# Optimization experiments

Measured on AMD Instinct MI355X. Metric: run time of the kernel, lower is better.

Reference implementation:

```python
import jax, jax.numpy as jnp
import numpy as np

D_IN = 2048
D_OUT = 2048
NUM_HEADS = 16
HEAD_DIM = D_OUT // NUM_HEADS
CONTEXT_LENGTH = 4096
THETA_BASE = 10000.0


def _rope_tables(seq_len):
    half = HEAD_DIM // 2
    inv_freq = 1.0 / (THETA_BASE ** (jnp.arange(half, dtype=jnp.float32) / half))
    positions = jnp.arange(seq_len, dtype=jnp.float32)
    angles = positions[:, None] * inv_freq[None, :]          # [S, half]
    angles = jnp.concatenate([angles, angles], axis=-1)      # [S, HEAD_DIM]
    return jnp.cos(angles), jnp.sin(angles)


def _apply_rope(x, cos, sin):
    # x: [B, H, S, D]
    half = x.shape[-1] // 2
    x1, x2 = x[..., :half], x[..., half:]
    rotated = jnp.concatenate([-x2, x1], axis=-1)
    return x * cos[None, None, :, :] + rotated * sin[None, None, :, :]


def setup_inputs() -> dict:
    key = jax.random.key(0)
    ks = jax.random.split(key, 5)
    x = jax.random.normal(ks[0], (1, 4096, D_IN), dtype=jnp.float32)
    scale_in = 1.0 / np.sqrt(D_IN)
    scale_out = 1.0 / np.sqrt(D_OUT)
    w_q = jax.random.normal(ks[1], (D_OUT, D_IN), dtype=jnp.float32) * scale_in
    w_k = jax.random.normal(ks[2], (D_OUT, D_IN), dtype=jnp.float32) * scale_in
    w_v = jax.random.normal(ks[3], (D_OUT, D_IN), dtype=jnp.float32) * scale_in
    w_o = jax.random.normal(ks[4], (D_IN, D_OUT), dtype=jnp.float32) * scale_out
    return {"x": x, "w_q": w_q, "w_k": w_k, "w_v": w_v, "w_o": w_o}


def reference(x, w_q, w_k, w_v, w_o):
    b, s, _ = x.shape
    cos, sin = _rope_tables(s)

    def split_heads(t):  # [B,S,D_OUT] -> [B,H,S,HEAD_DIM]
        return t.reshape(b, s, NUM_HEADS, HEAD_DIM).transpose(0, 2, 1, 3)

    q = split_heads(jnp.einsum('bsd,od->bso', x, w_q))
    k = split_heads(jnp.einsum('bsd,od->bso', x, w_k))
    v = split_heads(jnp.einsum('bsd,od->bso', x, w_v))

    q = _apply_rope(q, cos, sin)
    k = _apply_rope(k, cos, sin)

    scores = jnp.einsum('bhqd,bhkd->bhqk', q, k) / jnp.sqrt(jnp.float32(HEAD_DIM))
    causal = jnp.tril(jnp.ones((s, s), dtype=bool))
    scores = jnp.where(causal[None, None, :, :], scores, -jnp.inf)
    attn = jax.nn.softmax(scores, axis=-1)

    ctx = jnp.einsum('bhqk,bhkd->bhqd', attn, v)  # [B,H,S,HEAD_DIM]
    ctx = ctx.transpose(0, 2, 1, 3).reshape(b, s, D_OUT)
    return jnp.einsum('bso,do->bsd', ctx, w_o)
```

## Files before the change

kernel.cpp:

```cpp
#include <hip/hip_runtime.h>
#include <hip/hip_bf16.h>
#include <stdint.h>

#define SEQ 4096
#define DM 2048
#define NH 16
#define HD 128

typedef __attribute__((ext_vector_type(4)))  float f32x4;
typedef __attribute__((ext_vector_type(16))) float f32x16;
typedef __attribute__((ext_vector_type(8)))  short bf16x8;
typedef __attribute__((ext_vector_type(4)))  float float4_t;
typedef __attribute__((ext_vector_type(4)))  short s16x4;
typedef __attribute__((ext_vector_type(2)))  int   i32x2;
typedef __attribute__((ext_vector_type(2)))  unsigned u32x2;

__device__ __forceinline__ short f2bf(float f) {
  union { float f; unsigned u; } c; c.f = f;
  unsigned u = c.u;
  u += 0x7FFFu + ((u >> 16) & 1u);
  return (short)(u >> 16);
}

__device__ __forceinline__ int cvtpk(float lo, float hi) {
  int r;
  asm("v_cvt_pk_bf16_f32 %0, %1, %2" : "=v"(r) : "v"(lo), "v"(hi));
  return r;
}

__device__ __forceinline__ void async16(const void* g, void* l) {
  __builtin_amdgcn_global_load_lds((const __attribute__((address_space(1))) void*)g,
                                   (__attribute__((address_space(3))) void*)l, 16, 0, 0);
}

__global__ __launch_bounds__(256) void rope_tables_kernel(float2* __restrict__ tab) {
  int idx = blockIdx.x * 256 + threadIdx.x;
  int s = idx >> 6, j = idx & 63;
  float invf = expf(-(float)j * (9.210340371976184f / 64.0f));
  float ang = (float)s * invf;
  tab[idx] = make_float2(cosf(ang), sinf(ang));
}

__global__ __launch_bounds__(256) void f32_to_bf16_kernel(const float* __restrict__ in,
                                                          short* __restrict__ out, int n4) {
  int stride = gridDim.x * 256;
  for (int i = blockIdx.x * 256 + threadIdx.x; i < n4; i += stride) {
    float4_t v = ((const float4_t*)in)[i];
    s16x4 r;
    #pragma unroll
    for (int u = 0; u < 4; u++) r[u] = f2bf(v[u]);
    ((s16x4*)out)[i] = r;
  }
}

template<int OUT_MODE>
__global__ __launch_bounds__(256) void gemm_async_kernel(
    const short* __restrict__ A, const short* __restrict__ B,
    void* __restrict__ Cp, int M, int N, int K) {
  __shared__ short As[128 * 64];
  __shared__ short Bs[128 * 64];
  const int t = threadIdx.x, lane = t & 63, w = t >> 6;
  const int wr = w >> 1, wc = w & 1;
  const size_t Mbase = (size_t)blockIdx.x * 128;
  const size_t Nbase = (size_t)blockIdx.y * 128;
  f32x4 acc[4][4] = {};

  for (int k0 = 0; k0 < K; k0 += 64) {
    __syncthreads();
    #pragma unroll
    for (int c = 0; c < 4; c++) {
      int ob = w * 4096 + c * 1024;
      int o = ob + lane * 16;
      int row = o >> 7;
      int cb = (o & 127) ^ ((row & 7) << 4);
      async16((const char*)A + ((Mbase + row) * (size_t)K + k0) * 2 + cb, (char*)As + ob);
      async16((const char*)B + ((Nbase + row) * (size_t)K + k0) * 2 + cb, (char*)Bs + ob);
    }
    __syncthreads();

    bf16x8 a[2][4], b[2][4];
    #pragma unroll
    for (int ks = 0; ks < 2; ks++) {
      #pragma unroll
      for (int m = 0; m < 4; m++) {
        int row = wr * 64 + m * 16 + (lane & 15);
        int chunk = ks * 64 + (lane >> 4) * 16;
        a[ks][m] = *(const bf16x8*)((const char*)As + row * 128 + (chunk ^ ((row & 7) << 4)));
      }
      #pragma unroll
      for (int n = 0; n < 4; n++) {
        int row = wc * 64 + n * 16 + (lane & 15);
        int chunk = ks * 64 + (lane >> 4) * 16;
        b[ks][n] = *(const bf16x8*)((const char*)Bs + row * 128 + (chunk ^ ((row & 7) << 4)));
      }
    }
    #pragma unroll
    for (int ks = 0; ks < 2; ks++)
      #pragma unroll
      for (int m = 0; m < 4; m++)
        #pragma unroll
        for (int n = 0; n < 4; n++)
          acc[m][n] = __builtin_amdgcn_mfma_f32_16x16x32_bf16(a[ks][m], b[ks][n], acc[m][n], 0, 0, 0);
  }

  #pragma unroll
  for (int m = 0; m < 4; m++)
    #pragma unroll
    for (int n = 0; n < 4; n++)
      #pragma unroll
      for (int j = 0; j < 4; j++) {
        size_t row = Mbase + wr * 64 + m * 16 + (lane >> 4) * 4 + j;
        size_t col = Nbase + wc * 64 + n * 16 + (lane & 15);
        float v = acc[m][n][j];
        if (OUT_MODE == 0) ((float*)Cp)[row * N + col] = v;
        else               ((short*)Cp)[col * (size_t)M + row] = f2bf(v);
      }
}

template<int IS_Q>
__global__ __launch_bounds__(256) void gemm_rope_kernel(
    const short* __restrict__ A, const short* __restrict__ B,
    short* __restrict__ C, const float2* __restrict__ tab) {
  __shared__ short As[128 * 64];
  __shared__ short Bs[128 * 64];
  const int t = threadIdx.x, lane = t & 63, w = t >> 6;
  const size_t Mbase = (size_t)blockIdx.x * 128;
  const size_t Nbase = (size_t)blockIdx.y * 128;
  const int K = DM;
  f32x4 acc[2][8] = {};

  for (int k0 = 0; k0 < K; k0 += 64) {
    __syncthreads();
    #pragma unroll
    for (int c = 0; c < 4; c++) {
      int ob = w * 4096 + c * 1024;
      int o = ob + lane * 16;
      int row = o >> 7;
      int cb = (o & 127) ^ ((row & 7) << 4);
      async16((const char*)A + ((Mbase + row) * (size_t)K + k0) * 2 + cb, (char*)As + ob);
      async16((const char*)B + ((Nbase + row) * (size_t)K + k0) * 2 + cb, (char*)Bs + ob);
    }
    __syncthreads();

    bf16x8 a[2][2], b[2][8];
    #pragma unroll
    for (int ks = 0; ks < 2; ks++) {
      #pragma unroll
      for (int m = 0; m < 2; m++) {
        int row = w * 32 + m * 16 + (lane & 15);
        int chunk = ks * 64 + (lane >> 4) * 16;
        a[ks][m] = *(const bf16x8*)((const char*)As + row * 128 + (chunk ^ ((row & 7) << 4)));
      }
      #pragma unroll
      for (int n = 0; n < 8; n++) {
        int row = n * 16 + (lane & 15);
        int chunk = ks * 64 + (lane >> 4) * 16;
        b[ks][n] = *(const bf16x8*)((const char*)Bs + row * 128 + (chunk ^ ((row & 7) << 4)));
      }
    }
    #pragma unroll
    for (int ks = 0; ks < 2; ks++)
      #pragma unroll
      for (int m = 0; m < 2; m++)
        #pragma unroll
        for (int n = 0; n < 8; n++)
          acc[m][n] = __builtin_amdgcn_mfma_f32_16x16x32_bf16(a[ks][m], b[ks][n], acc[m][n], 0, 0, 0);
  }

  const float SC = IS_Q ? 0.12751746f : 1.0f;
  #pragma unroll
  for (int m = 0; m < 2; m++)
    #pragma unroll
    for (int n = 0; n < 4; n++)
      #pragma unroll
      for (int j = 0; j < 4; j++) {
        int row = (int)Mbase + w * 32 + m * 16 + (lane >> 4) * 4 + j;
        int dj = n * 16 + (lane & 15);
        float2 cs = tab[row * 64 + dj];
        float cc = cs.x * SC, ss = cs.y * SC;
        float r1 = acc[m][n][j], r2 = acc[m][n + 4][j];
        C[(size_t)row * DM + Nbase + dj]      = f2bf(r1 * cc - r2 * ss);
        C[(size_t)row * DM + Nbase + dj + 64] = f2bf(r2 * cc + r1 * ss);
      }
}

__global__ __launch_bounds__(512) void flash_attn4_kernel(
    const short* __restrict__ Q, const short* __restrict__ K,
    const short* __restrict__ VT, short* __restrict__ O) {
  __shared__ __align__(16) char LB[132096];
  const int t = threadIdx.x, lane = t & 63, w = t >> 6;
  const int hi = lane >> 5, c31 = lane & 31;
  const int s = w & 3, v = w >> 2;
  const int id = blockIdx.x;
  const int h  = (id & 7) * 2 + ((id >> 3) & 1);
  const int pr = id >> 4;

  float* Opart = (float*)LB;
  float* ml    = (float*)(LB + 131072);

  auto stage = [&](int kt, int buf) {
    #pragma unroll
    for (int it = 0; it < 4; it++) {
      const int ob = w * 4096 + it * 1024;
      const int o  = ob + lane * 16;
      const int row = o >> 8;
      const int xs = (o & 255) ^ ((row & 15) << 4);
      async16((const char*)K + ((size_t)(kt * 128 + row) * DM + h * HD) * 2 + xs,
              LB + buf * 32768 + ob);
      async16((const char*)VT + ((size_t)(h * HD + row) * SEQ + (size_t)kt * 128) * 2 + xs,
              LB + 65536 + buf * 32768 + ob);
    }
  };

  for (int rep = 0; rep < 2; rep++) {
    const int qt = rep ? (31 - pr) : pr;
    const int q0 = qt * 128;
    const int nt = qt + 1;
    const int qrow = q0 + s * 32 + c31;

    __syncthreads();
    stage(0, 0);

    bf16x8 qf[8];
    #pragma unroll
    for (int ss = 0; ss < 8; ss++)
      qf[ss] = *(const bf16x8*)(Q + (size_t)qrow * DM + h * HD + ss * 16 + hi * 8);

    f32x16 oacc[4] = {};
    float m = -3.0e38f, l = 0.f;

    __syncthreads();

    for (int kt = 0; kt < nt; kt++) {
      const int buf = kt & 1;
      if (kt + 1 < nt) stage(kt + 1, buf ^ 1);

      if (kt * 128 + v * 64 <= q0 + s * 32 + 31) {
        const char* KsB = LB + buf * 32768;
        const char* VsB = LB + 65536 + buf * 32768;

        f32x16 sacc[2] = {};
        __builtin_amdgcn_s_setprio(1);
        #pragma unroll
        for (int a = 0; a < 2; a++)
          #pragma unroll
          for (int ss = 0; ss < 8; ss++) {
            int row = v * 64 + a * 32 + c31;
            bf16x8 kf = *(const bf16x8*)(KsB + row * 256
                                         + ((ss * 32 + hi * 16) ^ ((row & 15) << 4)));
            sacc[a] = __builtin_amdgcn_mfma_f32_32x32x16_bf16(kf, qf[ss], sacc[a], 0, 0, 0);
          }
        __builtin_amdgcn_s_setprio(0);

        float t0[16];
        #pragma unroll
        for (int r = 0; r < 16; r++) t0[r] = fmaxf(sacc[0][r], sacc[1][r]);
        #pragma unroll
        for (int d = 8; d > 0; d >>= 1)
          #pragma unroll
          for (int r = 0; r < 8; r++) if (r < d) t0[r] = fmaxf(t0[r], t0[r + d]);
        float mx = t0[0];
        i32x2 mm = __builtin_amdgcn_permlane32_swap(__float_as_int(mx), __float_as_int(mx),
                                                    false, false);
        mx = fmaxf(__int_as_float(mm.x), __int_as_float(mm.y));

        if (__any(mx > m + 11.5416f)) {
          float mn = fmaxf(m, mx);
          float al = exp2f(m - mn);
          m = mn; l *= al;
          #pragma unroll
          for (int g = 0; g < 4; g++)
            #pragma unroll
            for (int r = 0; r < 16; r++) oacc[g][r] *= al;
        }

        const int rel = qrow - kt * 128 - v * 64;
        const bool maskT = (kt * 128 + v * 64 + 63) > (q0 + s * 32);
        #pragma unroll
        for (int a = 0; a < 2; a++)
          #pragma unroll
          for (int r = 0; r < 16; r++) {
            float e = exp2f(sacc[a][r] - m);
            if (maskT) {
              int kl = a * 32 + (r & 3) + 8 * (r >> 2) + 4 * hi;
              e = (kl > rel) ? 0.f : e;
            }
            sacc[a][r] = e;
          }

        float s0[16];
        #pragma unroll
        for (int r = 0; r < 16; r++) s0[r] = sacc[0][r] + sacc[1][r];
        #pragma unroll
        for (int d = 8; d > 0; d >>= 1)
          #pragma unroll
          for (int r = 0; r < 8; r++) if (r < d) s0[r] = s0[r] + s0[r + d];
        l += s0[0];

        bf16x8 pa[4];
        #pragma unroll
        for (int a = 0; a < 2; a++)
          #pragma unroll
          for (int sg = 0; sg < 2; sg++) {
            int q0a = cvtpk(sacc[a][8 * sg + 0], sacc[a][8 * sg + 1]);
            int q1a = cvtpk(sacc[a][8 * sg + 2], sacc[a][8 * sg + 3]);
            int q0b = cvtpk(sacc[a][8 * sg + 4], sacc[a][8 * sg + 5]);
            int q1b = cvtpk(sacc[a][8 * sg + 6], sacc[a][8 * sg + 7]);
            i32x2 r0 = __builtin_amdgcn_permlane32_swap(q0a, q0b, false, false);
            i32x2 r1 = __builtin_amdgcn_permlane32_swap(q1a, q1b, false, false);
            union { int d[4]; bf16x8 vv; } u;
            u.d[0] = r0.x; u.d[1] = r1.x; u.d[2] = r0.y; u.d[3] = r1.y;
            pa[a * 2 + sg] = u.vv;
          }

        __builtin_amdgcn_s_setprio(1);
        #pragma unroll
        for (int ks = 0; ks < 4; ks++)
          #pragma unroll
          for (int g = 0; g < 4; g++) {
            int row = g * 32 + c31;
            bf16x8 vf = *(const bf16x8*)(VsB + row * 256
                         + (((v * 64 + ks * 16 + hi * 8) * 2) ^ ((row & 15) << 4)));
            oacc[g] = __builtin_amdgcn_mfma_f32_32x32x16_bf16(vf, pa[ks], oacc[g], 0, 0, 0);
          }
        __builtin_amdgcn_s_setprio(0);
      }
      __syncthreads();
    }

    i32x2 lr = __builtin_amdgcn_permlane32_swap(__float_as_int(l), __float_as_int(l),
                                                false, false);
    l = __int_as_float(lr.x) + __int_as_float(lr.y);

    if (v == 1) {
      #pragma unroll
      for (int g = 0; g < 4; g++)
        #pragma unroll
        for (int r = 0; r < 16; r++) {
          int d = g * 32 + (r & 3) + 8 * (r >> 2) + 4 * hi;
          Opart[s * 4096 + d * 32 + c31] = oacc[g][r];
        }
      if (hi == 0) {
        ml[(s * 32 + c31) * 2]     = m;
        ml[(s * 32 + c31) * 2 + 1] = l;
      }
    }
    __syncthreads();
    if (v == 0) {
      float lB = ml[(s * 32 + c31) * 2 + 1];
      float mB = (lB > 0.f) ? ml[(s * 32 + c31) * 2] : -3.0e38f;
      float ms = fmaxf(m, mB);
      float aA = exp2f(m - ms), aB = exp2f(mB - ms);
      float linv = 1.0f / (l * aA + lB * aB);
      float sA = aA * linv, sB = aB * linv;
      #pragma unroll
      for (int g = 0; g < 4; g++)
        #pragma unroll
        for (int tt = 0; tt < 4; tt++) {
          float o[4];
          #pragma unroll
          for (int e = 0; e < 4; e++) {
            int d = g * 32 + e + 8 * tt + 4 * hi;
            o[e] = oacc[g][4 * tt + e] * sA + Opart[s * 4096 + d * 32 + c31] * sB;
          }
          u32x2 pk;
          pk.x = (unsigned)cvtpk(o[0], o[1]);
          pk.y = (unsigned)cvtpk(o[2], o[3]);
          *(u32x2*)(O + (size_t)qrow * DM + h * HD + g * 32 + tt * 8 + hi * 4) = pk;
        }
    }
  }
}

extern "C" void kernel_launch(void* const* d_in, const int* in_sizes, int n_in,
                              void* d_out, int out_size, void* d_ws, size_t ws_size,
                              hipStream_t stream) {
  const float* x  = (const float*)d_in[0];
  const float* wq = (const float*)d_in[1];
  const float* wk = (const float*)d_in[2];
  const float* wv = (const float*)d_in[3];
  const float* wo = (const float*)d_in[4];
  float* out = (float*)d_out;

  const size_t SQDMs = (size_t)SEQ * DM;
  short* Qb   = (short*)d_ws;
  short* Kb   = Qb + SQDMs;
  short* VTb  = Kb + SQDMs;
  short* Cb   = VTb + SQDMs;
  short* xbf  = Cb + SQDMs;
  short* wbuf = xbf + SQDMs;
  float2* tab = (float2*)(wbuf + (size_t)DM * DM);

  rope_tables_kernel<<<SEQ * 64 / 256, 256, 0, stream>>>(tab);
  f32_to_bf16_kernel<<<2048, 256, 0, stream>>>(x, xbf, (int)(SQDMs / 4));

  dim3 g(SEQ / 128, DM / 128);
  f32_to_bf16_kernel<<<2048, 256, 0, stream>>>(wq, wbuf, DM * DM / 4);
  gemm_rope_kernel<1><<<g, 256, 0, stream>>>(xbf, wbuf, Qb, tab);
  f32_to_bf16_kernel<<<2048, 256, 0, stream>>>(wk, wbuf, DM * DM / 4);
  gemm_rope_kernel<0><<<g, 256, 0, stream>>>(xbf, wbuf, Kb, tab);
  f32_to_bf16_kernel<<<2048, 256, 0, stream>>>(wv, wbuf, DM * DM / 4);
  gemm_async_kernel<2><<<g, 256, 0, stream>>>(xbf, wbuf, VTb, SEQ, DM, DM);

  flash_attn4_kernel<<<256, 512, 0, stream>>>(Qb, Kb, VTb, Cb);

  f32_to_bf16_kernel<<<2048, 256, 0, stream>>>(wo, wbuf, DM * DM / 4);
  gemm_async_kernel<0><<<g, 256, 0, stream>>>(Cb, wbuf, out, SEQ, DM, DM);
}
```

Before: 315.5 us.

## Split attention KV tile across four wave groups with tree merge of partials

Attention blocks grow from 512 to 1024 threads, so each of four wave groups per Q slice handles 32 keys of the 128-key tile instead of two groups handling 64. Partial outputs are combined through a two-stage LDS tree reduction (publish/fold), and normalization moves to the end. exp2f is replaced by the hardware exp2 builtin. The aim is more waves per CU for latency hiding and finer causal skipping, at the cost of extra synchronization and merge work plus tighter register pressure under launch_bounds(1024).

```diff
diff --git a/kernel.cpp b/kernel.cpp
--- a/kernel.cpp
+++ b/kernel.cpp
@@ -26,6 +26,10 @@
   int r;
   asm("v_cvt_pk_bf16_f32 %0, %1, %2" : "=v"(r) : "v"(lo), "v"(hi));
   return r;
+}
+
+__device__ __forceinline__ float exp2r(float x) {
+  return __builtin_amdgcn_exp2f(x);
 }
 
 __device__ __forceinline__ void async16(const void* g, void* l) {
@@ -184,10 +188,10 @@
       }
 }
 
-__global__ __launch_bounds__(512) void flash_attn4_kernel(
+__global__ __launch_bounds__(1024, 4) void flash_attn5_kernel(
     const short* __restrict__ Q, const short* __restrict__ K,
     const short* __restrict__ VT, short* __restrict__ O) {
-  __shared__ __align__(16) char LB[132096];
+  __shared__ __align__(16) char LB[133120];
   const int t = threadIdx.x, lane = t & 63, w = t >> 6;
   const int hi = lane >> 5, c31 = lane & 31;
   const int s = w & 3, v = w >> 2;
@@ -195,20 +199,17 @@
   const int h  = (id & 7) * 2 + ((id >> 3) & 1);
   const int pr = id >> 4;
 
-  float* Opart = (float*)LB;
-  float* ml    = (float*)(LB + 131072);
-
   auto stage = [&](int kt, int buf) {
     #pragma unroll
-    for (int it = 0; it < 4; it++) {
-      const int ob = w * 4096 + it * 1024;
+    for (int it = 0; it < 2; it++) {
+      const int ob = w * 2048 + it * 1024;
       const int o  = ob + lane * 16;
       const int row = o >> 8;
       const int xs = (o & 255) ^ ((row & 15) << 4);
       async16((const char*)K + ((size_t)(kt * 128 + row) * DM + h * HD) * 2 + xs,
-              LB + buf * 32768 + ob);
+              LB + buf * 65536 + ob);
       async16((const char*)VT + ((size_t)(h * HD + row) * SEQ + (size_t)kt * 128) * 2 + xs,
-              LB + 65536 + buf * 32768 + ob);
+              LB + 32768 + buf * 65536 + ob);
     }
   };
 
@@ -235,30 +236,28 @@
       const int buf = kt & 1;
       if (kt + 1 < nt) stage(kt + 1, buf ^ 1);
 
-      if (kt * 128 + v * 64 <= q0 + s * 32 + 31) {
-        const char* KsB = LB + buf * 32768;
-        const char* VsB = LB + 65536 + buf * 32768;
-
-        f32x16 sacc[2] = {};
+      if (kt * 128 + v * 32 <= q0 + s * 32 + 31) {
+        const char* KsB = LB + buf * 65536;
+        const char* VsB = LB + 32768 + buf * 65536;
+
+        f32x16 sacc = {};
         __builtin_amdgcn_s_setprio(1);
         #pragma unroll
-        for (int a = 0; a < 2; a++)
+        for (int ss = 0; ss < 8; ss++) {
+          int row = v * 32 + c31;
+          bf16x8 kf = *(const bf16x8*)(KsB + row * 256
+                                       + ((ss * 32 + hi * 16) ^ ((row & 15) << 4)));
+          sacc = __builtin_amdgcn_mfma_f32_32x32x16_bf16(kf, qf[ss], sacc, 0, 0, 0);
+        }
+        __builtin_amdgcn_s_setprio(0);
+
+        float t0[8];
+        #pragma unroll
+        for (int r = 0; r < 8; r++) t0[r] = fmaxf(sacc[r], sacc[r + 8]);
+        #pragma unroll
+        for (int d = 4; d > 0; d >>= 1)
           #pragma unroll
-          for (int ss = 0; ss < 8; ss++) {
-            int row = v * 64 + a * 32 + c31;
-            bf16x8 kf = *(const bf16x8*)(KsB + row * 256
-                                         + ((ss * 32 + hi * 16) ^ ((row & 15) << 4)));
-            sacc[a] = __builtin_amdgcn_mfma_f32_32x32x16_bf16(kf, qf[ss], sacc[a], 0, 0, 0);
-          }
-        __builtin_amdgcn_s_setprio(0);
-
-        float t0[16];
-        #pragma unroll
-        for (int r = 0; r < 16; r++) t0[r] = fmaxf(sacc[0][r], sacc[1][r]);
-        #pragma unroll
-        for (int d = 8; d > 0; d >>= 1)
-          #pragma unroll
-          for (int r = 0; r < 8; r++) if (r < d) t0[r] = fmaxf(t0[r], t0[r + d]);
+          for (int r = 0; r < 4; r++) if (r < d) t0[r] = fmaxf(t0[r], t0[r + d]);
         float mx = t0[0];
         i32x2 mm = __builtin_amdgcn_permlane32_swap(__float_as_int(mx), __float_as_int(mx),
                                                     false, false);
@@ -266,7 +265,7 @@
 
         if (__any(mx > m + 11.5416f)) {
           float mn = fmaxf(m, mx);
-          float al = exp2f(m - mn);
+          float al = exp2r(m - mn);
           m = mn; l *= al;
           #pragma unroll
           for (int g = 0; g < 4; g++)
@@ -274,53 +273,49 @@
             for (int r = 0; r < 16; r++) oacc[g][r] *= al;
         }
 
-        const int rel = qrow - kt * 128 - v * 64;
-        const bool maskT = (kt * 128 + v * 64 + 63) > (q0 + s * 32);
-        #pragma unroll
-        for (int a = 0; a < 2; a++)
+        const int rel = qrow - kt * 128 - v * 32;
+        const bool maskT = (kt * 128 + v * 32 + 31) > (q0 + s * 32);
+        #pragma unroll
+        for (int r = 0; r < 16; r++) {
+          float e = exp2r(sacc[r] - m);
+          if (maskT) {
+            int kl = (r & 3) + 8 * (r >> 2) + 4 * hi;
+            e = (kl > rel) ? 0.f : e;
+          }
+          sacc[r] = e;
+        }
+
+        float s0[8];
+        #pragma unroll
+        for (int r = 0; r < 8; r++) s0[r] = sacc[r] + sacc[r + 8];
+        #pragma unroll
+        for (int d = 4; d > 0; d >>= 1)
           #pragma unroll
-          for (int r = 0; r < 16; r++) {
-            float e = exp2f(sacc[a][r] - m);
-            if (maskT) {
-              int kl = a * 32 + (r & 3) + 8 * (r >> 2) + 4 * hi;
-              e = (kl > rel) ? 0.f : e;
-            }
-            sacc[a][r] = e;
-          }
-
-        float s0[16];
-        #pragma unroll
-        for (int r = 0; r < 16; r++) s0[r] = sacc[0][r] + sacc[1][r];
-        #pragma unroll
-        for (int d = 8; d > 0; d >>= 1)
-          #pragma unroll
-          for (int r = 0; r < 8; r++) if (r < d) s0[r] = s0[r] + s0[r + d];
+          for (int r = 0; r < 4; r++) if (r < d) s0[r] = s0[r] + s0[r + d];
         l += s0[0];
 
-        bf16x8 pa[4];
-        #pragma unroll
-        for (int a = 0; a < 2; a++)
-          #pragma unroll
-          for (int sg = 0; sg < 2; sg++) {
-            int q0a = cvtpk(sacc[a][8 * sg + 0], sacc[a][8 * sg + 1]);
-            int q1a = cvtpk(sacc[a][8 * sg + 2], sacc[a][8 * sg + 3]);
-            int q0b = cvtpk(sacc[a][8 * sg + 4], sacc[a][8 * sg + 5]);
-            int q1b = cvtpk(sacc[a][8 * sg + 6], sacc[a][8 * sg + 7]);
-            i32x2 r0 = __builtin_amdgcn_permlane32_swap(q0a, q0b, false, false);
-            i32x2 r1 = __builtin_amdgcn_permlane32_swap(q1a, q1b, false, false);
-            union { int d[4]; bf16x8 vv; } u;
-            u.d[0] = r0.x; u.d[1] = r1.x; u.d[2] = r0.y; u.d[3] = r1.y;
-            pa[a * 2 + sg] = u.vv;
-          }
+        bf16x8 pa[2];
+        #pragma unroll
+        for (int sg = 0; sg < 2; sg++) {
+          int q0a = cvtpk(sacc[8 * sg + 0], sacc[8 * sg + 1]);
+          int q1a = cvtpk(sacc[8 * sg + 2], sacc[8 * sg + 3]);
+          int q0b = cvtpk(sacc[8 * sg + 4], sacc[8 * sg + 5]);
+          int q1b = cvtpk(sacc[8 * sg + 6], sacc[8 * sg + 7]);
+          i32x2 r0 = __builtin_amdgcn_permlane32_swap(q0a, q0b, false, false);
+          i32x2 r1 = __builtin_amdgcn_permlane32_swap(q1a, q1b, false, false);
+          union { int d[4]; bf16x8 vv; } u;
+          u.d[0] = r0.x; u.d[1] = r1.x; u.d[2] = r0.y; u.d[3] = r1.y;
+          pa[sg] = u.vv;
+        }
 
         __builtin_amdgcn_s_setprio(1);
         #pragma unroll
-        for (int ks = 0; ks < 4; ks++)
+        for (int ks = 0; ks < 2; ks++)
           #pragma unroll
           for (int g = 0; g < 4; g++) {
             int row = g * 32 + c31;
             bf16x8 vf = *(const bf16x8*)(VsB + row * 256
-                         + (((v * 64 + ks * 16 + hi * 8) * 2) ^ ((row & 15) << 4)));
+                         + ((v * 64 + ks * 32 + hi * 16) ^ ((row & 15) << 4)));
             oacc[g] = __builtin_amdgcn_mfma_f32_32x32x16_bf16(vf, pa[ks], oacc[g], 0, 0, 0);
           }
         __builtin_amdgcn_s_setprio(0);
@@ -332,40 +327,53 @@
                                                 false, false);
     l = __int_as_float(lr.x) + __int_as_float(lr.y);
 
-    if (v == 1) {
+    auto publish = [&](int r) {
+      float* Op = (float*)(LB + r * 65536) + s * 4096;
       #pragma unroll
       for (int g = 0; g < 4; g++)
         #pragma unroll
-        for (int r = 0; r < 16; r++) {
-          int d = g * 32 + (r & 3) + 8 * (r >> 2) + 4 * hi;
-          Opart[s * 4096 + d * 32 + c31] = oacc[g][r];
+        for (int rr = 0; rr < 16; rr++) {
+          int d = g * 32 + (rr & 3) + 8 * (rr >> 2) + 4 * hi;
+          Op[d * 32 + c31] = oacc[g][rr];
         }
       if (hi == 0) {
-        ml[(s * 32 + c31) * 2]     = m;
-        ml[(s * 32 + c31) * 2 + 1] = l;
-      }
-    }
+        float* mm2 = (float*)(LB + 131072 + r * 1024) + (s * 32 + c31) * 2;
+        mm2[0] = m; mm2[1] = l;
+      }
+    };
+    auto fold = [&](int r) {
+      const float* mm2 = (const float*)(LB + 131072 + r * 1024) + (s * 32 + c31) * 2;
+      float lB = mm2[1];
+      float mB = (lB > 0.f) ? mm2[0] : -3.0e38f;
+      float ms = fmaxf(m, mB);
+      float aA = exp2r(m - ms), aB = exp2r(mB - ms);
+      const float* Op = (const float*)(LB + r * 65536) + s * 4096;
+      #pragma unroll
+      for (int g = 0; g < 4; g++)
+        #pragma unroll
+        for (int rr = 0; rr < 16; rr++) {
+          int d = g * 32 + (rr & 3) + 8 * (rr >> 2) + 4 * hi;
+          oacc[g][rr] = oacc[g][rr] * aA + Op[d * 32 + c31] * aB;
+        }
+      m = ms; l = l * aA + lB * aB;
+    };
+
+    if (v & 1) publish(v >> 1);
+    __syncthreads();
+    if (!(v & 1)) fold(v >> 1);
+    __syncthreads();
+    if (v == 2) publish(0);
     __syncthreads();
     if (v == 0) {
-      float lB = ml[(s * 32 + c31) * 2 + 1];
-      float mB = (lB > 0.f) ? ml[(s * 32 + c31) * 2] : -3.0e38f;
-      float ms = fmaxf(m, mB);
-      float aA = exp2f(m - ms), aB = exp2f(mB - ms);
-      float linv = 1.0f / (l * aA + lB * aB);
-      float sA = aA * linv, sB = aB * linv;
+      fold(0);
+      float inv = 1.0f / l;
       #pragma unroll
       for (int g = 0; g < 4; g++)
         #pragma unroll
         for (int tt = 0; tt < 4; tt++) {
-          float o[4];
-          #pragma unroll
-          for (int e = 0; e < 4; e++) {
-            int d = g * 32 + e + 8 * tt + 4 * hi;
-            o[e] = oacc[g][4 * tt + e] * sA + Opart[s * 4096 + d * 32 + c31] * sB;
-          }
           u32x2 pk;
-          pk.x = (unsigned)cvtpk(o[0], o[1]);
-          pk.y = (unsigned)cvtpk(o[2], o[3]);
+          pk.x = (unsigned)cvtpk(oacc[g][4 * tt + 0] * inv, oacc[g][4 * tt + 1] * inv);
+          pk.y = (unsigned)cvtpk(oacc[g][4 * tt + 2] * inv, oacc[g][4 * tt + 3] * inv);
           *(u32x2*)(O + (size_t)qrow * DM + h * HD + g * 32 + tt * 8 + hi * 4) = pk;
         }
     }
@@ -402,7 +410,7 @@
   f32_to_bf16_kernel<<<2048, 256, 0, stream>>>(wv, wbuf, DM * DM / 4);
   gemm_async_kernel<2><<<g, 256, 0, stream>>>(xbf, wbuf, VTb, SEQ, DM, DM);
 
-  flash_attn4_kernel<<<256, 512, 0, stream>>>(Qb, Kb, VTb, Cb);
+  flash_attn5_kernel<<<256, 1024, 0, stream>>>(Qb, Kb, VTb, Cb);
 
   f32_to_bf16_kernel<<<2048, 256, 0, stream>>>(wo, wbuf, DM * DM / 4);
   gemm_async_kernel<0><<<g, 256, 0, stream>>>(Cb, wbuf, out, SEQ, DM, DM);
```

Result: slower. 463.1 us (+46.8%).
